# Kernel tuning notes

Measured on AMD Instinct MI355X. Metric: run time of the kernel, lower is better.

Reference implementation:

```python
import jax, jax.numpy as jnp
import numpy as np

H = 400   # hidden_size
V = 77    # vocab / window size
K = 10    # attention mixture components
OUT = 121
B, T, U = 64, 600, 50


def setup_inputs() -> dict:
    key = jax.random.key(0)
    ks = jax.random.split(key, 16)
    def p(k, shape, s=0.08):
        return jax.random.normal(k, shape, dtype=jnp.float32) * s
    # bias for kappa-increment chunk kept negative so kappa advances ~exp(-3)=0.05/step
    b_win = jnp.concatenate([jnp.zeros(2 * K, jnp.float32), jnp.full((K,), -3.0, jnp.float32)])
    return {
        "inputs": jax.random.normal(ks[0], (B, T, 3), dtype=jnp.float32),
        "text": jax.random.randint(ks[1], (B, U), 0, V),
        "text_mask": jnp.ones((B, U), jnp.float32),
        "h0": jnp.zeros((3, B, H), jnp.float32),
        "c0": jnp.zeros((3, B, H), jnp.float32),
        "prev_window_vec": jnp.zeros((B, 1, V), jnp.float32),
        "prev_kappa": jnp.zeros((B, K, 1), jnp.float32),
        "w_ih1": p(ks[2], (4 * H, 3 + V)), "w_hh1": p(ks[3], (4 * H, H)),
        "b_ih1": jnp.zeros((4 * H,), jnp.float32), "b_hh1": jnp.zeros((4 * H,), jnp.float32),
        "w_ih2": p(ks[4], (4 * H, 3 + V + H)), "w_hh2": p(ks[5], (4 * H, H)),
        "b_ih2": jnp.zeros((4 * H,), jnp.float32), "b_hh2": jnp.zeros((4 * H,), jnp.float32),
        "w_ih3": p(ks[6], (4 * H, 3 + V + H)), "w_hh3": p(ks[7], (4 * H, H)),
        "b_ih3": jnp.zeros((4 * H,), jnp.float32), "b_hh3": jnp.zeros((4 * H,), jnp.float32),
        "w_win": p(ks[8], (3 * K, H), 0.01), "b_win": b_win,
        "w_out": p(ks[9], (OUT, 3 * H)), "b_out": jnp.zeros((OUT,), jnp.float32),
    }


def lstm_cell(x, h, c, Wih, Whh, bih, bhh):
    # PyTorch gate order: i, f, g, o
    g = x @ Wih.T + bih + h @ Whh.T + bhh
    i, f, gg, o = jnp.split(g, 4, axis=-1)
    c = jax.nn.sigmoid(f) * c + jax.nn.sigmoid(i) * jnp.tanh(gg)
    h = jax.nn.sigmoid(o) * jnp.tanh(c)
    return h, c


def reference(inputs, text, text_mask, h0, c0, prev_window_vec, prev_kappa,
              w_ih1, w_hh1, b_ih1, b_hh1, w_ih2, w_hh2, b_ih2, b_hh2,
              w_ih3, w_hh3, b_ih3, b_hh3, w_win, b_win, w_out, b_out):
    enc = jax.nn.one_hot(text, V, dtype=jnp.float32)            # [B,U,V]
    u = jnp.arange(U, dtype=jnp.float32)                         # [U]

    def step1(carry, x_t):
        h, c, wv, kappa = carry                                  # h,c:[B,H] wv:[B,V] kappa:[B,K]
        xi = jnp.concatenate([x_t, wv], axis=-1)                 # [B,3+V]
        h, c = lstm_cell(xi, h, c, w_ih1, w_hh1, b_ih1, b_hh1)
        mix = jnp.exp(h @ w_win.T + b_win)                       # [B,3K]
        alpha, beta, dk = jnp.split(mix, 3, axis=-1)             # each [B,K]
        kappa = kappa + dk
        phi = jnp.sum(alpha[:, :, None] * jnp.exp(-beta[:, :, None] * (kappa[:, :, None] - u) ** 2), axis=1)  # [B,U]
        phi = phi * text_mask
        wv = jnp.einsum('bu,buv->bv', phi, enc)                  # [B,V]
        return (h, c, wv, kappa), (h, wv)

    carry0 = (h0[0], c0[0], prev_window_vec[:, 0, :], prev_kappa[:, :, 0])
    (h1, c1, _, kappa_last), (hid1, wvec) = jax.lax.scan(step1, carry0, jnp.swapaxes(inputs, 0, 1))
    hid1 = jnp.swapaxes(hid1, 0, 1)                              # [B,T,H]
    wvec = jnp.swapaxes(wvec, 0, 1)                              # [B,T,V]

    def run_lstm(x, h, c, Wih, Whh, bih, bhh):
        def step(carry, x_t):
            h, c = carry
            h, c = lstm_cell(x_t, h, c, Wih, Whh, bih, bhh)
            return (h, c), h
        _, hs = jax.lax.scan(step, (h, c), jnp.swapaxes(x, 0, 1))
        return jnp.swapaxes(hs, 0, 1)

    hid2 = run_lstm(jnp.concatenate([inputs, hid1, wvec], axis=-1), h0[1], c0[1], w_ih2, w_hh2, b_ih2, b_hh2)
    hid3 = run_lstm(jnp.concatenate([inputs, hid2, wvec], axis=-1), h0[2], c0[2], w_ih3, w_hh3, b_ih3, b_hh3)
    y_hat = jnp.concatenate([hid1, hid2, hid3], axis=-1) @ w_out.T + b_out  # [B,T,121]
    return y_hat, wvec, kappa_last[:, :, None]
```

## Files before the change

kernel.cpp:

```cpp
#include <hip/hip_runtime.h>
#include <cstdint>
#include <cstddef>
#include <cstring>

using u32 = unsigned int;
typedef _Float16 h2 __attribute__((ext_vector_type(2)));
typedef _Float16 h4 __attribute__((ext_vector_type(4)));
typedef _Float16 h8 __attribute__((ext_vector_type(8)));
typedef float f32x4 __attribute__((ext_vector_type(4)));

constexpr int B_=64, T_=600, U_=50, V_=77, H_=400, OUT_=121;
constexpr int G1=50, GPA=16, G2=50, G3=50, GOUT=8;
constexpr int NBLK = G1+GPA+G2+G3+GOUT;
constexpr u32 CNT0=50, CNT1=16, CNT2=50, CNT3=50;

constexpr size_t FLAGS_B = 0;
constexpr size_t FLAGS_SZ = 4ull*600*64;
constexpr size_t W1WG   = 15ull*32*4*8;
constexpr size_t W1F_B  = FLAGS_SZ;
constexpr size_t W2WG   = 28ull*32*4*8;
constexpr size_t W2F_B  = W1F_B + 50ull*W1WG*2;
constexpr size_t W3F_B  = W2F_B + 50ull*W2WG*2;
constexpr size_t WOWG   = 300ull*32*16;
constexpr size_t WOF_B  = W3F_B + 50ull*W2WG*2;
constexpr size_t WWFWG  = 200ull*32;
constexpr size_t WWF_B  = WOF_B + 8ull*WOWG*2;
constexpr size_t FWV_B  = WWF_B + 16ull*WWFWG*4;
constexpr size_t FH1_B  = FWV_B + 600ull*64*40*4;
constexpr size_t FH2_B  = FH1_B + 600ull*64*200*4;
constexpr size_t FH3_B  = FH2_B + 600ull*64*200*4;

constexpr int SW1 = 184;
constexpr int SW2 = 232;
constexpr int SWO = 244;
constexpr int SMEM_BYTES = 59392;

struct P {
  const float *x, *tmask, *h0, *c0, *pwv, *pkap;
  const int *text;
  const float *wih1,*whh1,*bih1,*bhh1;
  const float *wih2,*whh2,*bih2,*bhh2;
  const float *wih3,*whh3,*bih3,*bhh3;
  const float *wwin,*bwin,*wout,*bout;
  float *out_y,*out_wv,*out_kap;
  _Float16 *w1f,*w2f,*w3f,*wof;
  u32 *wwf;
  u32 *fwv,*fh1,*fh2,*fh3;
  u32 *flags;
};

__device__ __forceinline__ u32 ldc_u(const u32* p) {
  return __hip_atomic_load((u32*)p, __ATOMIC_RELAXED, __HIP_MEMORY_SCOPE_AGENT);
}
__device__ __forceinline__ void stc_u(u32* p, u32 v) {
  __hip_atomic_store(p, v, __ATOMIC_RELAXED, __HIP_MEMORY_SCOPE_AGENT);
}
__device__ __forceinline__ float sigm(float x) { return 1.f/(1.f+__expf(-x)); }
__device__ __forceinline__ h2 pk16(float a, float b) {
  auto t = __builtin_amdgcn_cvt_pkrtz(a, b);
  h2 r; memcpy(&r, &t, 4); return r;
}
__device__ __forceinline__ u32 h2u(h2 v) { u32 r; memcpy(&r, &v, 4); return r; }
__device__ __forceinline__ h2 u2h(u32 v) { h2 r; memcpy(&r, &v, 4); return r; }
__device__ __forceinline__ u32 pkf(float a, float b) { return h2u(pk16(a, b)); }
__device__ __forceinline__ float dot2(h2 a, h2 b, float c) { return __builtin_amdgcn_fdot2(a, b, c, false); }
__device__ __forceinline__ h2 lo4(h4 v) { return __builtin_shufflevector(v, v, 0, 1); }
__device__ __forceinline__ h2 hi4(h4 v) { return __builtin_shufflevector(v, v, 2, 3); }

__device__ __forceinline__ void wait_cnt(u32* cnt, int stage, int t, u32 target) {
  if (threadIdx.x == 0) {
    const u32* s = cnt + ((size_t)stage*600 + t)*16;
    while (ldc_u(s) < target) {}
  }
  __syncthreads();
}
__device__ __forceinline__ void add_cnt(u32* cnt, int stage, int t) {
  if (threadIdx.x == 0)
    (void)__hip_atomic_fetch_add(cnt + ((size_t)stage*600 + t)*16, 1u,
                                 __ATOMIC_RELAXED, __HIP_MEMORY_SCOPE_AGENT);
}

__device__ __forceinline__ void mfma_chunk5(const _Float16* pan, int SWf, const _Float16* WA,
                                            int w, int l, f32x4& acc0, f32x4& acc1) {
  const _Float16* bp0 = pan + ((w>>1)*32 + (l&15))*SWf + (l>>4)*8;
  const _Float16* bp1 = bp0 + 16*SWf;
  const _Float16* ap  = WA + (((16*(w&1) + (l&15))*4) + (l>>4))*8;
#pragma unroll
  for (int ks = 0; ks < 5; ++ks) {
    h8 a  = *(const h8*)(ap  + ks*1024);
    h8 b0 = *(const h8*)(bp0 + ks*32);
    h8 b1 = *(const h8*)(bp1 + ks*32);
    acc0 = __builtin_amdgcn_mfma_f32_16x16x32_f16(a, b0, acc0, 0, 0, 0);
    acc1 = __builtin_amdgcn_mfma_f32_16x16x32_f16(a, b1, acc1, 0, 0, 0);
  }
}
__device__ __forceinline__ void mfma_chunk7(const _Float16* pan, int SWf, const _Float16* WA,
                                            int w, int l, f32x4& acc0, f32x4& acc1) {
  const _Float16* bp0 = pan + ((w>>1)*32 + (l&15))*SWf + (l>>4)*8;
  const _Float16* bp1 = bp0 + 16*SWf;
  const _Float16* ap  = WA + (((16*(w&1) + (l&15))*4) + (l>>4))*8;
#pragma unroll
  for (int ks = 0; ks < 7; ++ks) {
    h8 a  = *(const h8*)(ap  + ks*1024);
    h8 b0 = *(const h8*)(bp0 + ks*32);
    h8 b1 = *(const h8*)(bp1 + ks*32);
    acc0 = __builtin_amdgcn_mfma_f32_16x16x32_f16(a, b0, acc0, 0, 0, 0);
    acc1 = __builtin_amdgcn_mfma_f32_16x16x32_f16(a, b1, acc1, 0, 0, 0);
  }
}

__device__ void lstm1_role(const P& p, int wg, char* smem) {
  const int tid = threadIdx.x;
  const int w = tid >> 6, l = tid & 63;
  const int ul = (w&1)*4 + (l>>4);
  const int u  = wg*8 + ul;
  const int bA = (w>>1)*32 + (l&15), bB = bA + 16;
  _Float16* panA = (_Float16*)smem;
  _Float16* panB = panA + 64*SW1;
  _Float16* wgW = p.w1f + (size_t)wg * W1WG;
  for (int e = tid; e < 15360; e += 256) {
    int i = e & 7, q = (e>>3)&3, row = (e>>5)&31, ks = e>>10;
    int k = ks*32 + q*8 + i;
    int cu = row>>2, g = row&3;
    int r = g*400 + wg*8 + cu;
    float v;
    if (k < 400)      v = p.whh1[(size_t)r*400 + k];
    else if (k < 477) v = p.wih1[(size_t)r*80 + 3 + (k-400)];
    else              v = p.wih1[(size_t)r*80 + (k-477)];
    wgW[e] = (_Float16)v;
  }
  float bsum[4];
#pragma unroll
  for (int g = 0; g < 4; ++g) bsum[g] = p.bih1[g*400+u] + p.bhh1[g*400+u];
  float creg[2];
  creg[0] = p.c0[(size_t)bA*H_ + u];
  creg[1] = p.c0[(size_t)bB*H_ + u];
  __syncthreads();

  for (int t = 0; t < T_; ++t) {
    f32x4 acc0 = {0.f,0.f,0.f,0.f}, acc1 = {0.f,0.f,0.f,0.f};
    if (t > 0) wait_cnt(p.flags, 0, t-1, CNT0); else __syncthreads();
    const u32* h1p = p.fh1 + (size_t)(t-1)*64*200;
    {
      u32 tmp[20];
#pragma unroll
      for (int it = 0; it < 20; ++it) {
        int idx = tid + it*256; int b = idx/80, q = idx - b*80;
        if (t == 0) { float2 f = *(const float2*)(p.h0 + (size_t)b*H_ + 2*q); tmp[it] = pkf(f.x, f.y); }
        else tmp[it] = h1p[b*200 + q];
      }
#pragma unroll
      for (int it = 0; it < 20; ++it) {
        int idx = tid + it*256; int b = idx/80, q = idx - b*80;
        ((u32*)panA)[b*92 + q] = tmp[it];
      }
    }
    __syncthreads();
    {
      u32 tmp[20];
#pragma unroll
      for (int it = 0; it < 20; ++it) {
        int idx = tid + it*256; int b = idx/80, q = 80 + (idx - b*80);
        if (t == 0) { float2 f = *(const float2*)(p.h0 + (size_t)b*H_ + 2*q); tmp[it] = pkf(f.x, f.y); }
        else tmp[it] = h1p[b*200 + q];
      }
      mfma_chunk5(panA, SW1, wgW, w, l, acc0, acc1);
#pragma unroll
      for (int it = 0; it < 20; ++it) {
        int idx = tid + it*256; int b = idx/80, q = idx - b*80;
        ((u32*)panB)[b*92 + q] = tmp[it];
      }
    }
    __syncthreads();
    {
      u32 tmp[10];
#pragma unroll
      for (int it = 0; it < 10; ++it) {
        int idx = tid + it*256; int b = idx/40, q = idx - b*40;
        if (t == 0) { float2 f = *(const float2*)(p.h0 + (size_t)b*H_ + 2*(160+q)); tmp[it] = pkf(f.x, f.y); }
        else tmp[it] = h1p[b*200 + 160 + q];
      }
      mfma_chunk5(panB, SW1, wgW + 5*1024, w, l, acc0, acc1);
#pragma unroll
      for (int it = 0; it < 10; ++it) {
        int idx = tid + it*256; int b = idx/40, q = idx - b*40;
        ((u32*)panA)[b*92 + q] = tmp[it];
      }
    }
    if (t > 0) wait_cnt(p.flags, 1, t-1, CNT1); else __syncthreads();
    {
      u32 tmp[10];
#pragma unroll
      for (int it = 0; it < 10; ++it) {
        int idx = tid + it*256; int b = idx/40, q = idx - b*40;
        u32 v;
        if (q < 38) {
          if (t == 0) v = pkf(p.pwv[(size_t)b*V_ + 2*q], p.pwv[(size_t)b*V_ + 2*q + 1]);
          else v = p.fwv[((size_t)(t-1)*64 + b)*40 + q];
        } else if (q == 38) {
          float wv76 = (t == 0) ? p.pwv[(size_t)b*V_ + 76]
                                : (float)u2h(p.fwv[((size_t)(t-1)*64 + b)*40 + 38]).x;
          v = pkf(wv76, p.x[((size_t)b*T_ + t)*3 + 0]);
        } else {
          v = pkf(p.x[((size_t)b*T_ + t)*3 + 1], p.x[((size_t)b*T_ + t)*3 + 2]);
        }
        tmp[it] = v;
      }
#pragma unroll
      for (int it = 0; it < 10; ++it) {
        int idx = tid + it*256; int b = idx/40, q = idx - b*40;
        ((u32*)panA)[b*92 + 40 + q] = tmp[it];
      }
    }
    __syncthreads();
    mfma_chunk5(panA, SW1, wgW + 10*1024, w, l, acc0, acc1);

    float hA, hB;
    {
      float cn = sigm(acc0[1]+bsum[1])*creg[0] + sigm(acc0[0]+bsum[0])*tanhf(acc0[2]+bsum[2]);
      creg[0] = cn; hA = sigm(acc0[3]+bsum[3])*tanhf(cn);
      float cn2 = sigm(acc1[1]+bsum[1])*creg[1] + sigm(acc1[0]+bsum[0])*tanhf(acc1[2]+bsum[2]);
      creg[1] = cn2; hB = sigm(acc1[3]+bsum[3])*tanhf(cn2);
    }
    {
      float hAp = __shfl_xor(hA, 16, 64);
      float hBp = __shfl_xor(hB, 16, 64);
      if (((l>>4) & 1) == 0) {
        const int pi = wg*4 + (ul>>1);
        stc_u(p.fh1 + ((size_t)t*64 + bA)*200 + pi, pkf(hA, hAp));
        stc_u(p.fh1 + ((size_t)t*64 + bB)*200 + pi, pkf(hB, hBp));
      }
    }
    __syncthreads();
    add_cnt(p.flags, 0, t);
  }
}

__device__ void pa_role(const P& p, int pa, char* smem) {
  const int tid = threadIdx.x;
  const int b0p = pa*4;
  u32* hsm    = (u32*)smem;
  float* mixP = (float*)(smem + 3200);
  float* mixL = (float*)(smem + 4160);
  float* kapL = (float*)(smem + 4640);
  float* wvs  = (float*)(smem + 4800);
  int* textL  = (int*)(smem + 6032);
  u32* wwf = p.wwf + (size_t)pa * WWFWG;
  for (int e = tid; e < 200*30; e += 256) {
    int kk = e / 30, m = e - (e/30)*30;
    wwf[(size_t)kk*32 + m] = pkf(p.wwin[(size_t)m*400 + 2*kk], p.wwin[(size_t)m*400 + 2*kk + 1]);
  }
  for (int i = tid; i < 200; i += 256)
    textL[i] = p.text[(size_t)(b0p + i/50)*U_ + (i - (i/50)*50)];
  float kap_reg = 0.f;
  if (tid < 120 && (tid % 30) >= 20)
    kap_reg = p.pkap[(size_t)(b0p + tid/30)*10 + (tid % 30 - 20)];
  __syncthreads();

  for (int t = 0; t < T_; ++t) {
    wait_cnt(p.flags, 0, t, CNT0);
    for (int e = tid; e < 800; e += 256) {
      int bl = e / 200, q = e - bl*200;
      hsm[e] = p.fh1[((size_t)t*64 + b0p + bl)*200 + q];
    }
    for (int i = tid; i < 308; i += 256) wvs[i] = 0.f;
    __syncthreads();
    if (tid < 240) {
      int pp = tid >> 1, h = tid & 1;
      int bl = pp / 30, m = pp - bl*30;
      const u32* hp = hsm + bl*200 + h*100;
      const u32* wp = wwf + (size_t)(h*100)*32 + m;
      float d0=0.f, d1=0.f, d2=0.f, d3=0.f;
#pragma unroll 4
      for (int kk = 0; kk < 100; kk += 4) {
        d0 = dot2(u2h(hp[kk]),   u2h(wp[(size_t)kk*32]),     d0);
        d1 = dot2(u2h(hp[kk+1]), u2h(wp[(size_t)(kk+1)*32]), d1);
        d2 = dot2(u2h(hp[kk+2]), u2h(wp[(size_t)(kk+2)*32]), d2);
        d3 = dot2(u2h(hp[kk+3]), u2h(wp[(size_t)(kk+3)*32]), d3);
      }
      mixP[tid] = (d0+d1)+(d2+d3);
    }
    __syncthreads();
    if (tid < 120) {
      int bl = tid / 30, m = tid - bl*30;
      float v = __expf(mixP[2*tid] + mixP[2*tid+1] + p.bwin[m]);
      mixL[tid] = v;
      if (m >= 20) {
        kap_reg += v;
        kapL[bl*10 + (m-20)] = kap_reg;
        if (t == T_-1) p.out_kap[(size_t)(b0p+bl)*10 + (m-20)] = kap_reg;
      }
    }
    __syncthreads();
    if (tid < 200) {
      int bl = tid / 50, uu = tid - bl*50;
      const float fu = (float)uu;
      float s = 0.f;
#pragma unroll
      for (int k = 0; k < 10; ++k) {
        float df = kapL[bl*10+k] - fu;
        s += mixL[bl*30+k] * __expf(-mixL[bl*30+10+k]*df*df);
      }
      s *= p.tmask[(size_t)(b0p+bl)*U_ + uu];
      atomicAdd(&wvs[bl*77 + textL[tid]], s);
    }
    __syncthreads();
    for (int i = tid; i < 308; i += 256) {
      int bl = i / 77, v = i - (i/77)*77;
      p.out_wv[((size_t)(b0p+bl)*T_ + t)*V_ + v] = wvs[i];
    }
    for (int i = tid; i < 160; i += 256) {
      int bl = i / 40, pr = i - (i/40)*40;
      int b = b0p + bl;
      float f0, f1;
      if (pr < 38)       { f0 = wvs[bl*77 + 2*pr]; f1 = wvs[bl*77 + 2*pr + 1]; }
      else if (pr == 38) { f0 = wvs[bl*77 + 76];   f1 = p.x[((size_t)b*T_ + t)*3 + 0]; }
      else               { f0 = p.x[((size_t)b*T_ + t)*3 + 1]; f1 = p.x[((size_t)b*T_ + t)*3 + 2]; }
      stc_u(p.fwv + ((size_t)t*64 + b)*40 + pr, pkf(f0, f1));
    }
    __syncthreads();
    add_cnt(p.flags, 1, t);
  }
}

__device__ __forceinline__ void stage_l23(u32* pan, int tid, int ph, int t,
    const u32* fwvt, const u32* hint, const u32* rect, const float* h0f) {
  u32 tmp[28];
#pragma unroll
  for (int it = 0; it < 28; ++it) {
    int idx = tid + it*256;
    int b = idx/112, pl = idx - b*112;
    int gp = ph*112 + pl;
    u32 v;
    if (gp < 40) v = fwvt[b*40 + gp];
    else if (gp < 240) v = hint[b*200 + gp - 40];
    else if (gp < 440) {
      if (t == 0) { float2 f = *(const float2*)(h0f + (size_t)b*H_ + 2*(gp-240)); v = pkf(f.x, f.y); }
      else v = rect[b*200 + gp - 240];
    } else v = 0u;
    tmp[it] = v;
  }
#pragma unroll
  for (int it = 0; it < 28; ++it) {
    int idx = tid + it*256;
    int b = idx/112, pl = idx - b*112;
    pan[b*116 + pl] = tmp[it];
  }
}

template <int L>
__device__ void lstm_role(const P& p, int wg, char* smem) {
  const int tid = threadIdx.x;
  const int w = tid >> 6, l = tid & 63;
  const int ul = (w&1)*4 + (l>>4);
  const int u  = wg*8 + ul;
  const int bA = (w>>1)*32 + (l&15), bB = bA + 16;
  constexpr int STG = (L==2) ? 2 : 3;
  _Float16* wgW = ((L==2) ? p.w2f : p.w3f) + (size_t)wg * W2WG;
  const float* wih = (L==2) ? p.wih2 : p.wih3;
  const float* whh = (L==2) ? p.whh2 : p.whh3;
  const float* bih = (L==2) ? p.bih2 : p.bih3;
  const float* bhh = (L==2) ? p.bhh2 : p.bhh3;
  const u32* hin = (L==2) ? p.fh1 : p.fh2;
  u32* rec = (L==2) ? p.fh2 : p.fh3;
  _Float16* panA = (_Float16*)smem;
  _Float16* panB = panA + 64*SW2;

  for (int e = tid; e < 28672; e += 256) {
    int i = e & 7, q = (e>>3)&3, row = (e>>5)&31, ks = e>>10;
    int k = ks*32 + q*8 + i;
    int cu = row>>2, g = row&3;
    int r = g*400 + wg*8 + cu;
    float v;
    if (k < 77)       v = wih[(size_t)r*480 + 403 + k];
    else if (k < 80)  v = wih[(size_t)r*480 + (k-77)];
    else if (k < 480) v = wih[(size_t)r*480 + 3 + (k-80)];
    else if (k < 880) v = whh[(size_t)r*400 + (k-480)];
    else              v = 0.f;
    wgW[e] = (_Float16)v;
  }
  float bsum[4];
#pragma unroll
  for (int g = 0; g < 4; ++g) bsum[g] = bih[g*400+u] + bhh[g*400+u];
  float creg[2];
  creg[0] = p.c0[(size_t)(L-1)*B_*H_ + (size_t)bA*H_ + u];
  creg[1] = p.c0[(size_t)(L-1)*B_*H_ + (size_t)bB*H_ + u];
  __syncthreads();

  for (int t = 0; t < T_; ++t) {
    f32x4 acc0 = {0.f,0.f,0.f,0.f}, acc1 = {0.f,0.f,0.f,0.f};
    if (L == 2) wait_cnt(p.flags, 1, t, CNT1);
    else        wait_cnt(p.flags, 2, t, CNT2);
    const u32* fwvt = p.fwv + (size_t)t*64*40;
    const u32* hint = hin + (size_t)t*64*200;
    const u32* rect = rec + (size_t)(t-1)*64*200;
    const float* h0f = p.h0 + (size_t)(L-1)*B_*H_;
    stage_l23((u32*)panA, tid, 0, t, fwvt, hint, rect, h0f);
    __syncthreads();
    {
      u32 tmp[28];
#pragma unroll
      for (int it = 0; it < 28; ++it) {
        int idx = tid + it*256;
        int b = idx/112, pl = idx - b*112;
        tmp[it] = hint[b*200 + 72 + pl];
      }
      mfma_chunk7(panA, SW2, wgW, w, l, acc0, acc1);
#pragma unroll
      for (int it = 0; it < 28; ++it) {
        int idx = tid + it*256;
        int b = idx/112, pl = idx - b*112;
        ((u32*)panB)[b*116 + pl] = tmp[it];
      }
    }
    if (t > 0) wait_cnt(p.flags, STG, t-1, CNT2); else __syncthreads();
    {
      u32 tmp[28];
#pragma unroll
      for (int it = 0; it < 28; ++it) {
        int idx = tid + it*256;
        int b = idx/112, pl = idx - b*112;
        int gp = 224 + pl;
        u32 v;
        if (gp < 240) v = hint[b*200 + gp - 40];
        else if (t == 0) { float2 f = *(const float2*)(h0f + (size_t)b*H_ + 2*(gp-240)); v = pkf(f.x, f.y); }
        else v = rect[b*200 + gp - 240];
        tmp[it] = v;
      }
      mfma_chunk7(panB, SW2, wgW + 7*1024, w, l, acc0, acc1);
#pragma unroll
      for (int it = 0; it < 28; ++it) {
        int idx = tid + it*256;
        int b = idx/112, pl = idx - b*112;
        ((u32*)panA)[b*116 + pl] = tmp[it];
      }
    }
    __syncthreads();
    {
      u32 tmp[28];
#pragma unroll
      for (int it = 0; it < 28; ++it) {
        int idx = tid + it*256;
        int b = idx/112, pl = idx - b*112;
        int gp = 336 + pl;
        u32 v;
        if (gp < 440) {
          if (t == 0) { float2 f = *(const float2*)(h0f + (size_t)b*H_ + 2*(gp-240)); v = pkf(f.x, f.y); }
          else v = rect[b*200 + gp - 240];
        } else v = 0u;
        tmp[it] = v;
      }
      mfma_chunk7(panA, SW2, wgW + 14*1024, w, l, acc0, acc1);
#pragma unroll
      for (int it = 0; it < 28; ++it) {
        int idx = tid + it*256;
        int b = idx/112, pl = idx - b*112;
        ((u32*)panB)[b*116 + pl] = tmp[it];
      }
    }
    __syncthreads();
    mfma_chunk7(panB, SW2, wgW + 21*1024, w, l, acc0, acc1);

    float hA, hB;
    {
      float cn = sigm(acc0[1]+bsum[1])*creg[0] + sigm(acc0[0]+bsum[0])*tanhf(acc0[2]+bsum[2]);
      creg[0] = cn; hA = sigm(acc0[3]+bsum[3])*tanhf(cn);
      float cn2 = sigm(acc1[1]+bsum[1])*creg[1] + sigm(acc1[0]+bsum[0])*tanhf(acc1[2]+bsum[2]);
      creg[1] = cn2; hB = sigm(acc1[3]+bsum[3])*tanhf(cn2);
    }
    {
      float hAp = __shfl_xor(hA, 16, 64);
      float hBp = __shfl_xor(hB, 16, 64);
      if (((l>>4) & 1) == 0) {
        const int pi = wg*4 + (ul>>1);
        stc_u(rec + ((size_t)t*64 + bA)*200 + pi, pkf(hA, hAp));
        stc_u(rec + ((size_t)t*64 + bB)*200 + pi, pkf(hB, hBp));
      }
    }
    __syncthreads();
    add_cnt(p.flags, STG, t);
  }
}

__device__ void out_role(const P& p, int g, char* smem) {
  const int tid = threadIdx.x;
  const int cg = tid & 31, bg = tid >> 5;
  const int c0 = cg*4;
  _Float16* pan = (_Float16*)smem;
  _Float16* wofg = p.wof + (size_t)g*WOWG;
  for (int e = tid; e < 300*32*16; e += 256) {
    int kk = e >> 9, rem = e & 511;
    int cgi = rem >> 4, j4 = rem & 15;
    int j = j4 >> 2, kc = j4 & 3;
    int c = cgi*4 + j; if (c > 120) c = 120;
    wofg[e] = (_Float16)p.wout[(size_t)c*1200 + kk*4 + kc];
  }
  float bo[4];
#pragma unroll
  for (int j = 0; j < 4; ++j) {
    int c = c0 + j; if (c > 120) c = 120;
    bo[j] = p.bout[c];
  }
  __syncthreads();

  for (int t = g; t < T_; t += GOUT) {
    wait_cnt(p.flags, 3, t, CNT3);
    float acc[8][4];
#pragma unroll
    for (int r = 0; r < 8; ++r)
#pragma unroll
      for (int j = 0; j < 4; ++j) acc[r][j] = 0.f;

    for (int ph = 0; ph < 5; ++ph) {
      for (int idx = tid; idx < 7680; idx += 256) {
        int b = idx / 120, pl = idx - b*120;
        int Pp = ph*120 + pl;
        u32 pv;
        if (Pp < 200)      pv = p.fh1[((size_t)t*64 + b)*200 + Pp];
        else if (Pp < 400) pv = p.fh2[((size_t)t*64 + b)*200 + (Pp-200)];
        else               pv = p.fh3[((size_t)t*64 + b)*200 + (Pp-400)];
        ((u32*)pan)[b*122 + pl] = pv;
      }
      __syncthreads();
      const _Float16* wp = wofg + ((size_t)(ph*60)*32 + cg)*16;
#pragma unroll 3
      for (int k = 0; k < 240; k += 4) {
        h4 wa = *(const h4*)(wp);
        h4 wb = *(const h4*)(wp+4);
        h4 wc = *(const h4*)(wp+8);
        h4 wd = *(const h4*)(wp+12);
        wp += 512;
#pragma unroll
        for (int r = 0; r < 8; ++r) {
          h4 a = *(const h4*)(pan + (bg*8+r)*SWO + k);
          h2 al = lo4(a), ah = hi4(a);
          acc[r][0] = dot2(al, lo4(wa), acc[r][0]); acc[r][0] = dot2(ah, hi4(wa), acc[r][0]);
          acc[r][1] = dot2(al, lo4(wb), acc[r][1]); acc[r][1] = dot2(ah, hi4(wb), acc[r][1]);
          acc[r][2] = dot2(al, lo4(wc), acc[r][2]); acc[r][2] = dot2(ah, hi4(wc), acc[r][2]);
          acc[r][3] = dot2(al, lo4(wd), acc[r][3]); acc[r][3] = dot2(ah, hi4(wd), acc[r][3]);
        }
      }
      __syncthreads();
    }
#pragma unroll
    for (int r = 0; r < 8; ++r)
#pragma unroll
      for (int j = 0; j < 4; ++j) {
        int c = c0 + j;
        if (c < 121)
          p.out_y[((size_t)(bg*8+r)*T_ + t)*OUT_ + c] = acc[r][j] + bo[j];
      }
    __syncthreads();
  }
}

__global__ __launch_bounds__(256) void hw_pipeline(P p) {
  __shared__ __align__(16) char smem_raw[SMEM_BYTES];
  const int bid = blockIdx.x;
  if (bid < G1) lstm1_role(p, bid, smem_raw);
  else if (bid < G1+GPA) pa_role(p, bid - G1, smem_raw);
  else if (bid < G1+GPA+G2) lstm_role<2>(p, bid - G1 - GPA, smem_raw);
  else if (bid < G1+GPA+G2+G3) lstm_role<3>(p, bid - G1 - GPA - G2, smem_raw);
  else out_role(p, bid - G1 - GPA - G2 - G3, smem_raw);
}

extern "C" void kernel_launch(void* const* d_in, const int* in_sizes, int n_in,
                              void* d_out, int out_size, void* d_ws, size_t ws_size,
                              hipStream_t stream) {
  (void)in_sizes; (void)n_in; (void)out_size; (void)ws_size;
  P p;
  p.x = (const float*)d_in[0];
  p.text = (const int*)d_in[1];
  p.tmask = (const float*)d_in[2];
  p.h0 = (const float*)d_in[3];
  p.c0 = (const float*)d_in[4];
  p.pwv = (const float*)d_in[5];
  p.pkap = (const float*)d_in[6];
  p.wih1 = (const float*)d_in[7];  p.whh1 = (const float*)d_in[8];
  p.bih1 = (const float*)d_in[9];  p.bhh1 = (const float*)d_in[10];
  p.wih2 = (const float*)d_in[11]; p.whh2 = (const float*)d_in[12];
  p.bih2 = (const float*)d_in[13]; p.bhh2 = (const float*)d_in[14];
  p.wih3 = (const float*)d_in[15]; p.whh3 = (const float*)d_in[16];
  p.bih3 = (const float*)d_in[17]; p.bhh3 = (const float*)d_in[18];
  p.wwin = (const float*)d_in[19]; p.bwin = (const float*)d_in[20];
  p.wout = (const float*)d_in[21]; p.bout = (const float*)d_in[22];
  float* out = (float*)d_out;
  p.out_y  = out;
  p.out_wv = out + (size_t)B_*T_*OUT_;
  p.out_kap = p.out_wv + (size_t)B_*T_*V_;
  char* ws = (char*)d_ws;
  p.flags = (u32*)(ws + FLAGS_B);
  p.w1f = (_Float16*)(ws + W1F_B);
  p.w2f = (_Float16*)(ws + W2F_B);
  p.w3f = (_Float16*)(ws + W3F_B);
  p.wof = (_Float16*)(ws + WOF_B);
  p.wwf = (u32*)(ws + WWF_B);
  p.fwv = (u32*)(ws + FWV_B);
  p.fh1 = (u32*)(ws + FH1_B);
  p.fh2 = (u32*)(ws + FH2_B);
  p.fh3 = (u32*)(ws + FH3_B);
  (void)hipMemsetAsync(ws + FLAGS_B, 0, FLAGS_SZ, stream);
  hipLaunchKernelGGL(hw_pipeline, dim3(NBLK), dim3(256), 0, stream, p);
}
```

Measured before the change: 15.51 ms.

## Recompute attention window redundantly in each LSTM1 block to drop cross-block wait

```diff
diff --git a/kernel.cpp b/kernel.cpp
--- a/kernel.cpp
+++ b/kernel.cpp
@@ -25,7 +25,9 @@
 constexpr size_t WOF_B  = W3F_B + 50ull*W2WG*2;
 constexpr size_t WWFWG  = 200ull*32;
 constexpr size_t WWF_B  = WOF_B + 8ull*WOWG*2;
-constexpr size_t FWV_B  = WWF_B + 16ull*WWFWG*4;
+constexpr size_t WWMWG  = 15ull*32*4*8;
+constexpr size_t WWM_B  = WWF_B + 16ull*WWFWG*4;
+constexpr size_t FWV_B  = WWM_B + 50ull*WWMWG*2;
 constexpr size_t FH1_B  = FWV_B + 600ull*64*40*4;
 constexpr size_t FH2_B  = FH1_B + 600ull*64*200*4;
 constexpr size_t FH3_B  = FH2_B + 600ull*64*200*4;
@@ -43,7 +45,7 @@
   const float *wih3,*whh3,*bih3,*bhh3;
   const float *wwin,*bwin,*wout,*bout;
   float *out_y,*out_wv,*out_kap;
-  _Float16 *w1f,*w2f,*w3f,*wof;
+  _Float16 *w1f,*w2f,*w3f,*wof,*wwm;
   u32 *wwf;
   u32 *fwv,*fh1,*fh2,*fh3;
   u32 *flags;
@@ -117,7 +119,11 @@
   const int bA = (w>>1)*32 + (l&15), bB = bA + 16;
   _Float16* panA = (_Float16*)smem;
   _Float16* panB = panA + 64*SW1;
+  float* kapS = (float*)(smem + 47104);
+  float* mixE = (float*)(smem + 49664);
+  float* wvs  = (float*)(smem + 23552);
   _Float16* wgW = p.w1f + (size_t)wg * W1WG;
+  _Float16* wgM = p.wwm + (size_t)wg * WWMWG;
   for (int e = tid; e < 15360; e += 256) {
     int i = e & 7, q = (e>>3)&3, row = (e>>5)&31, ks = e>>10;
     int k = ks*32 + q*8 + i;
@@ -129,6 +135,14 @@
     else              v = p.wih1[(size_t)r*80 + (k-477)];
     wgW[e] = (_Float16)v;
   }
+  for (int e = tid; e < 15360; e += 256) {
+    int i = e & 7, q = (e>>3)&3, row = (e>>5)&31, ks = e>>10;
+    int k = ks*32 + q*8 + i;
+    float v = 0.f;
+    if (row < 30 && k < 400) v = p.wwin[(size_t)row*400 + k];
+    wgM[e] = (_Float16)v;
+  }
+  for (int i = tid; i < 640; i += 256) kapS[i] = p.pkap[i];
   float bsum[4];
 #pragma unroll
   for (int g = 0; g < 4; ++g) bsum[g] = p.bih1[g*400+u] + p.bhh1[g*400+u];
@@ -139,6 +153,7 @@
 
   for (int t = 0; t < T_; ++t) {
     f32x4 acc0 = {0.f,0.f,0.f,0.f}, acc1 = {0.f,0.f,0.f,0.f};
+    f32x4 am0  = {0.f,0.f,0.f,0.f}, am1  = {0.f,0.f,0.f,0.f};
     if (t > 0) wait_cnt(p.flags, 0, t-1, CNT0); else __syncthreads();
     const u32* h1p = p.fh1 + (size_t)(t-1)*64*200;
     {
@@ -165,6 +180,7 @@
         else tmp[it] = h1p[b*200 + q];
       }
       mfma_chunk5(panA, SW1, wgW, w, l, acc0, acc1);
+      if (t > 0) mfma_chunk5(panA, SW1, wgM, w, l, am0, am1);
 #pragma unroll
       for (int it = 0; it < 20; ++it) {
         int idx = tid + it*256; int b = idx/80, q = idx - b*80;
@@ -173,46 +189,68 @@
     }
     __syncthreads();
     {
-      u32 tmp[10];
+      u32 tmp[10], tw[10];
 #pragma unroll
       for (int it = 0; it < 10; ++it) {
         int idx = tid + it*256; int b = idx/40, q = idx - b*40;
         if (t == 0) { float2 f = *(const float2*)(p.h0 + (size_t)b*H_ + 2*(160+q)); tmp[it] = pkf(f.x, f.y); }
         else tmp[it] = h1p[b*200 + 160 + q];
+        if (t == 0) {
+          u32 v;
+          if (q < 38)       v = pkf(p.pwv[(size_t)b*V_ + 2*q], p.pwv[(size_t)b*V_ + 2*q + 1]);
+          else if (q == 38) v = pkf(p.pwv[(size_t)b*V_ + 76], p.x[((size_t)b*T_ + t)*3 + 0]);
+          else              v = pkf(p.x[((size_t)b*T_ + t)*3 + 1], p.x[((size_t)b*T_ + t)*3 + 2]);
+          tw[it] = v;
+        } else tw[it] = 0u;
       }
       mfma_chunk5(panB, SW1, wgW + 5*1024, w, l, acc0, acc1);
+      if (t > 0) mfma_chunk5(panB, SW1, wgM + 5*1024, w, l, am0, am1);
 #pragma unroll
       for (int it = 0; it < 10; ++it) {
         int idx = tid + it*256; int b = idx/40, q = idx - b*40;
         ((u32*)panA)[b*92 + q] = tmp[it];
-      }
-    }
-    if (t > 0) wait_cnt(p.flags, 1, t-1, CNT1); else __syncthreads();
-    {
-      u32 tmp[10];
-#pragma unroll
-      for (int it = 0; it < 10; ++it) {
-        int idx = tid + it*256; int b = idx/40, q = idx - b*40;
+        ((u32*)panA)[b*92 + 40 + q] = tw[it];
+      }
+    }
+    __syncthreads();
+    if (t > 0) {
+      for (int i = tid; i < 4928; i += 256) wvs[i] = 0.f;
+      mfma_chunk5(panA, SW1, wgM + 10*1024, w, l, am0, am1);
+#pragma unroll
+      for (int r = 0; r < 4; ++r) {
+        int m = 16*(w&1) + (l>>4)*4 + r;
+        if (m < 30) {
+          float e0 = __expf(am0[r] + p.bwin[m]);
+          float e1 = __expf(am1[r] + p.bwin[m]);
+          mixE[bA*32 + m] = e0;
+          mixE[bB*32 + m] = e1;
+          if (m >= 20) { kapS[bA*10 + (m-20)] += e0; kapS[bB*10 + (m-20)] += e1; }
+        }
+      }
+      __syncthreads();
+      for (int c = tid; c < 3200; c += 256) {
+        int b = c/50, uu = c - (c/50)*50;
+        const float fu = (float)uu;
+        float s = 0.f;
+#pragma unroll
+        for (int k = 0; k < 10; ++k) {
+          float df = kapS[b*10+k] - fu;
+          s += mixE[b*32+k] * __expf(-mixE[b*32+10+k]*df*df);
+        }
+        s *= p.tmask[(size_t)b*U_ + uu];
+        atomicAdd(&wvs[b*77 + p.text[(size_t)b*U_ + uu]], s);
+      }
+      __syncthreads();
+      for (int i = tid; i < 2560; i += 256) {
+        int b = i/40, q = i - (i/40)*40;
         u32 v;
-        if (q < 38) {
-          if (t == 0) v = pkf(p.pwv[(size_t)b*V_ + 2*q], p.pwv[(size_t)b*V_ + 2*q + 1]);
-          else v = p.fwv[((size_t)(t-1)*64 + b)*40 + q];
-        } else if (q == 38) {
-          float wv76 = (t == 0) ? p.pwv[(size_t)b*V_ + 76]
-                                : (float)u2h(p.fwv[((size_t)(t-1)*64 + b)*40 + 38]).x;
-          v = pkf(wv76, p.x[((size_t)b*T_ + t)*3 + 0]);
-        } else {
-          v = pkf(p.x[((size_t)b*T_ + t)*3 + 1], p.x[((size_t)b*T_ + t)*3 + 2]);
-        }
-        tmp[it] = v;
-      }
-#pragma unroll
-      for (int it = 0; it < 10; ++it) {
-        int idx = tid + it*256; int b = idx/40, q = idx - b*40;
-        ((u32*)panA)[b*92 + 40 + q] = tmp[it];
-      }
-    }
-    __syncthreads();
+        if (q < 38)       v = pkf(wvs[b*77 + 2*q], wvs[b*77 + 2*q + 1]);
+        else if (q == 38) v = pkf(wvs[b*77 + 76], p.x[((size_t)b*T_ + t)*3 + 0]);
+        else              v = pkf(p.x[((size_t)b*T_ + t)*3 + 1], p.x[((size_t)b*T_ + t)*3 + 2]);
+        ((u32*)panA)[b*92 + 40 + q] = v;
+      }
+      __syncthreads();
+    }
     mfma_chunk5(panA, SW1, wgW + 10*1024, w, l, acc0, acc1);
 
     float hA, hB;
@@ -594,6 +632,7 @@
   p.w2f = (_Float16*)(ws + W2F_B);
   p.w3f = (_Float16*)(ws + W3F_B);
   p.wof = (_Float16*)(ws + WOF_B);
+  p.wwm = (_Float16*)(ws + WWM_B);
   p.wwf = (u32*)(ws + WWF_B);
   p.fwv = (u32*)(ws + FWV_B);
   p.fh1 = (u32*)(ws + FH1_B);
```

New measurement: 15.51 ms. No clear change (+0.0%).
